# Performance work log

Measured on AMD Instinct MI355X. Metric: run time of the kernel, lower is better.

Reference implementation:

```python
import jax, jax.numpy as jnp
import numpy as np

B = 128          # batch of IQ signals
L = 128          # signal length
PL = 16          # patch length
ST = 4           # patch stride
WIN = 4          # local window
NPATCH = (L - PL) // ST + 1   # 29
HID = 256
NCLS = 8
NG = B * NPATCH               # number of patch graphs
N = NG * PL                   # total nodes


def _build_edges():
    src, dst = [], []
    for i in range(PL):
        for j in range(PL):
            if 0 < abs(i - j) <= WIN:
                src.append(i); dst.append(j)
    bs = np.array(src, np.int32)          # [108]
    bd = np.array(dst, np.int32)
    off = (np.arange(NG, dtype=np.int32) * PL)[:, None]
    isrc = (off + bs[None, :]).reshape(-1)
    idst = (off + bd[None, :]).reshape(-1)
    # cross-patch edges: last node of patch p -> first node of patch p+1
    b = np.arange(B, dtype=np.int32)[:, None]
    p = np.arange(NPATCH - 1, dtype=np.int32)[None, :]
    csrc = (b * NPATCH * PL + p * PL + (PL - 1)).reshape(-1)
    cdst = (b * NPATCH * PL + (p + 1) * PL).reshape(-1)
    return np.concatenate([isrc, csrc]), np.concatenate([idst, cdst])


def setup_inputs() -> dict:
    key = jax.random.key(0)
    ks = jax.random.split(key, 10)
    s = 0.05
    esrc, edst = _build_edges()
    return {
        "iq_signal": jax.random.normal(ks[0], (B, 2, L), jnp.float32),
        "edge_src": jnp.asarray(esrc),
        "edge_dst": jnp.asarray(edst),
        # SAGEConv layer 0 (in=2): lin_l (agg, with bias), lin_r (root, no bias)
        "W0_agg": jax.random.normal(ks[1], (HID, 2), jnp.float32) * s,
        "W0_root": jax.random.normal(ks[2], (HID, 2), jnp.float32) * s,
        "b0": jnp.zeros((HID,), jnp.float32),
        # SAGEConv layers 1..3 (256 -> 256), stacked
        "W_agg": jax.random.normal(ks[3], (3, HID, HID), jnp.float32) * s,
        "W_root": jax.random.normal(ks[4], (3, HID, HID), jnp.float32) * s,
        "b_lin": jnp.zeros((3, HID), jnp.float32),
        # per-layer LayerNorms
        "ln_scale": jnp.ones((4, HID), jnp.float32),
        "ln_bias": jnp.zeros((4, HID), jnp.float32),
        # classifier head
        "cls_W1": jax.random.normal(ks[5], (HID, HID), jnp.float32) * s,
        "cls_b1": jnp.zeros((HID,), jnp.float32),
        "cls_ln_scale": jnp.ones((HID,), jnp.float32),
        "cls_ln_bias": jnp.zeros((HID,), jnp.float32),
        "cls_W2": jax.random.normal(ks[6], (NCLS, HID), jnp.float32) * s,
        "cls_b2": jnp.zeros((NCLS,), jnp.float32),
    }


def _ln(x, g, b):
    m = x.mean(-1, keepdims=True)
    v = ((x - m) ** 2).mean(-1, keepdims=True)
    return (x - m) * jax.lax.rsqrt(v + 1e-5) * g + b


def reference(iq_signal, edge_src, edge_dst, W0_agg, W0_root, b0,
              W_agg, W_root, b_lin, ln_scale, ln_bias,
              cls_W1, cls_b1, cls_ln_scale, cls_ln_bias, cls_W2, cls_b2):
    # patch extraction: [B,2,L] -> [B,NPATCH,PL,2] -> node features [N,2]
    idx = jnp.arange(NPATCH)[:, None] * ST + jnp.arange(PL)[None, :]   # [29,16]
    x = jnp.transpose(iq_signal[:, :, idx], (0, 2, 3, 1)).reshape(-1, 2)

    # in-degree for mean aggregation (0 -> safe divide by 1)
    ones = jnp.ones((edge_dst.shape[0],), x.dtype)
    deg = jax.ops.segment_sum(ones, edge_dst, num_segments=N)
    inv_deg = 1.0 / jnp.maximum(deg, 1.0)

    def sage(h, Wa, Wr, b):
        # mean-aggregate neighbor messages, then lin_l(agg) + lin_r(h) + bias
        agg = jax.ops.segment_sum(h[edge_src], edge_dst, num_segments=N)
        agg = agg * inv_deg[:, None]
        return agg @ Wa.T + h @ Wr.T + b

    # layer 0 (2 -> 256): no residual (shape change)
    h = jax.nn.relu(_ln(sage(x, W0_agg, W0_root, b0), ln_scale[0], ln_bias[0]))
    # layers 1..3 with residual
    for l in range(3):
        hn = jax.nn.relu(_ln(sage(h, W_agg[l], W_root[l], b_lin[l]),
                             ln_scale[l + 1], ln_bias[l + 1]))
        h = h + hn

    node_emb = h                                  # [N, 256]
    # global_mean_pool per patch graph (16 consecutive nodes each)
    gf = node_emb.reshape(NG, PL, HID).mean(axis=1)   # [NG, 256]
    z = jax.nn.relu(_ln(gf @ cls_W1.T + cls_b1, cls_ln_scale, cls_ln_bias))
    logits = z @ cls_W2.T + cls_b2                # [NG, 8]
    return logits, gf, node_emb
```

## Files before the change

### kernel.cpp

```cpp
#include <hip/hip_runtime.h>
#include <hip/hip_bf16.h>

typedef __hip_bfloat16 bf16;
typedef unsigned short u16;
typedef unsigned int uint32;
typedef __attribute__((ext_vector_type(8))) short bf16x8;
typedef __attribute__((ext_vector_type(4))) float f32x4;

#define BATCH   128
#define LSIG    128
#define PL      16
#define ST      4
#define WIN     4
#define NPATCH  29
#define NG      (BATCH * NPATCH)
#define NNODE   (NG * PL)
#define HID     256
#define NCLS    8

#define IQ_OFF    0
#define W0A_OFF   32768
#define W0R_OFF   33280
#define B0_OFF    33792
#define BLIN_OFF  34048
#define LNS_OFF   34816
#define LNB_OFF   35840
#define W1T_OFF   36864
#define CB1_OFF   102400
#define CLNS_OFF  102656
#define CLNB_OFF  102912
#define CW2_OFF   103168
#define CB2_OFF   105216
#define CVT_TOTAL 105224

#define P_BYTE_OFF   4096
#define WB_BYTE_OFF  425984
#define A_BYTE_OFF   1216512
#define B_BYTE_OFF   1959936
#define GF_EOFF      (NG * NCLS)
#define EMB_EOFF     (NG * NCLS + NG * HID)

__device__ __forceinline__ float b2f(bf16 x) { return __bfloat162float(x); }
__device__ __forceinline__ float lof(uint32 u) { return __uint_as_float(u << 16); }
__device__ __forceinline__ float hif(uint32 u) { return __uint_as_float(u & 0xFFFF0000u); }
__device__ __forceinline__ float ldmix(const void* p, int i, int fl) {
  return fl ? ((const float*)p)[i] : __bfloat162float(((const bf16*)p)[i]);
}

__global__ __launch_bounds__(256) void detect_kernel(const u16* __restrict__ iq, int* flag) {
  __shared__ int sbig, snz;
  int t = threadIdx.x;
  if (t == 0) { sbig = 0; snz = 0; }
  __syncthreads();
  int big = 0, nz = 0;
  for (int e = t; e < 16384; e += 256) {
    u16 u = iq[2 * e];
    int ex = (u >> 7) & 0xFF;
    if (ex >= 0xC0) big++;
    if (u != 0) nz++;
  }
  atomicAdd(&sbig, big); atomicAdd(&snz, nz);
  __syncthreads();
  if (t == 0) *flag = (sbig > 4 || snz < 100) ? 1 : 0;
}

__global__ __launch_bounds__(256) void convert_params(
    const int* __restrict__ flag,
    const void* iq, const void* w0a, const void* w0r, const void* b0,
    const void* blin, const void* lns, const void* lnb,
    const void* cw1, const void* cb1, const void* clns, const void* clnb,
    const void* cw2, const void* cb2,
    float* __restrict__ P) {
  int idx = blockIdx.x * 256 + threadIdx.x;
  if (idx >= CVT_TOTAL) return;
  int fl = *flag;
  float v;
  if (idx < W0A_OFF)        v = ldmix(iq,  idx, fl);
  else if (idx < W0R_OFF)   v = ldmix(w0a, idx - W0A_OFF, fl);
  else if (idx < B0_OFF)    v = ldmix(w0r, idx - W0R_OFF, fl);
  else if (idx < BLIN_OFF)  v = ldmix(b0,  idx - B0_OFF, fl);
  else if (idx < LNS_OFF)   v = ldmix(blin, idx - BLIN_OFF, fl);
  else if (idx < LNB_OFF)   v = ldmix(lns, idx - LNS_OFF, fl);
  else if (idx < W1T_OFF)   v = ldmix(lnb, idx - LNB_OFF, fl);
  else if (idx < CB1_OFF) { int t2 = idx - W1T_OFF;
    v = ldmix(cw1, (t2 & 255) * 256 + (t2 >> 8), fl); }
  else if (idx < CLNS_OFF)  v = ldmix(cb1, idx - CB1_OFF, fl);
  else if (idx < CLNB_OFF)  v = ldmix(clns, idx - CLNS_OFF, fl);
  else if (idx < CW2_OFF)   v = ldmix(clnb, idx - CLNB_OFF, fl);
  else if (idx < CB2_OFF)   v = ldmix(cw2, idx - CW2_OFF, fl);
  else                      v = ldmix(cb2, idx - CB2_OFF, fl);
  P[idx] = v;
}

__global__ __launch_bounds__(256) void convert_wb(
    const int* __restrict__ flag, const void* wag, const void* wro, bf16* __restrict__ WB) {
  int idx = blockIdx.x * 256 + threadIdx.x;
  int fl = *flag;
  int l = idx >> 17, m = (idx >> 16) & 1, r = idx & 65535;
  const void* src = m ? wro : wag;
  WB[idx] = __float2bfloat16(ldmix(src, l * 65536 + r, fl));
}

__global__ __launch_bounds__(256) void layer0_kernel(
    const float* __restrict__ P, bf16* __restrict__ hout) {
  int g = blockIdx.x, f = threadIdx.x;
  int b = g / NPATCH, p = g % NPATCH;
  __shared__ float x_s[PL][2];
  __shared__ float xp_s[2];
  __shared__ float agg_s[PL][2];
  __shared__ float o_s[PL][HID];
  __shared__ float mv_s[PL][2];
  if (f < 32) { int j = f & 15, c = f >> 4;
    x_s[j][c] = P[IQ_OFF + (b * 2 + c) * LSIG + p * ST + j]; }
  if (f < 2) xp_s[f] = (p > 0) ? P[IQ_OFF + (b * 2 + f) * LSIG + (p - 1) * ST + PL - 1] : 0.f;
  __syncthreads();
  if (f < 32) { int j = f & 15, c = f >> 4;
    float s = 0.f;
    int lo = j - WIN < 0 ? 0 : j - WIN, hi = j + WIN > 15 ? 15 : j + WIN;
    for (int i = lo; i <= hi; ++i) if (i != j) s += x_s[i][c];
    int deg = (j < WIN ? j : WIN) + ((15 - j) < WIN ? (15 - j) : WIN);
    if (j == 0 && p > 0) { s += xp_s[c]; deg += 1; }
    agg_s[j][c] = s / (float)deg;
  }
  __syncthreads();
  float wa0 = P[W0A_OFF + f * 2], wa1 = P[W0A_OFF + f * 2 + 1];
  float wr0 = P[W0R_OFF + f * 2], wr1 = P[W0R_OFF + f * 2 + 1];
  float bb = P[B0_OFF + f];
#pragma unroll
  for (int j = 0; j < PL; ++j)
    o_s[j][f] = agg_s[j][0] * wa0 + agg_s[j][1] * wa1 + x_s[j][0] * wr0 + x_s[j][1] * wr1 + bb;
  __syncthreads();
  { int j = f >> 4, q = f & 15;
    float s = 0.f, s2 = 0.f;
#pragma unroll
    for (int i = 0; i < 16; ++i) { float v = o_s[j][q + 16 * i]; s += v; s2 += v * v; }
#pragma unroll
    for (int m = 8; m >= 1; m >>= 1) { s += __shfl_xor(s, m); s2 += __shfl_xor(s2, m); }
    if (q == 0) { float mean = s * (1.f / HID);
      float var = s2 * (1.f / HID) - mean * mean;
      mv_s[j][0] = mean; mv_s[j][1] = rsqrtf(var + 1e-5f); }
  }
  __syncthreads();
  float gl = P[LNS_OFF + f], bl = P[LNB_OFF + f];
#pragma unroll
  for (int j = 0; j < PL; ++j) {
    float v = (o_s[j][f] - mv_s[j][0]) * mv_s[j][1] * gl + bl;
    v = v > 0.f ? v : 0.f;
    hout[(size_t)(g * PL + j) * HID + f] = __float2bfloat16(v);
  }
}

#define MFMA_BF16 __builtin_amdgcn_mfma_f32_16x16x32_bf16
__global__ __launch_bounds__(256, 2) void sage_mfma(
    const bf16* __restrict__ hin,
    const bf16* __restrict__ Wa, const bf16* __restrict__ Wr,
    const float* __restrict__ bias,
    const float* __restrict__ lng, const float* __restrict__ lnb,
    bf16* __restrict__ hout) {
  int t = threadIdx.x;
  int w = t >> 6, l = t & 63, lr = l & 15, lg = l >> 4;
  int g0 = blockIdx.x * 4;
  size_t nbase = (size_t)g0 * PL;
  __shared__ uint32 h32[64 * 128];
  __shared__ uint32 a32[64 * 128];
  float* mvp = (float*)h32;
  const uint32* hinw = (const uint32*)hin;

  int colbase = w * 64;
  const bf16* waB = Wa + (colbase + lr) * HID + lg * 8;
  const bf16* wrB = Wr + (colbase + lr) * HID + lg * 8;
  bf16x8 wa0[2][8], wr0[2][8];
#pragma unroll
  for (int nt = 0; nt < 2; ++nt)
#pragma unroll
    for (int ks = 0; ks < 8; ++ks) {
      wa0[nt][ks] = *(const bf16x8*)(waB + nt * 16 * HID + ks * 32);
      wr0[nt][ks] = *(const bf16x8*)(wrB + nt * 16 * HID + ks * 32);
    }

  const uint32* hg = hinw + nbase * 128;
#pragma unroll
  for (int it = 0; it < 8; ++it) {
    int u = it * 256 + t;
    int row = u >> 5, sl = u & 31;
    int sw = sl ^ (row & 7);
    *(uint4*)&h32[row * 128 + sw * 4] = *(const uint4*)(hg + u * 4);
  }
  __syncthreads();

  {
    int c2 = t & 127, Ph = t >> 7;
#pragma unroll
    for (int pi = 0; pi < 2; ++pi) {
      int pp = Ph + pi * 2;
      int pr = pp * 16;
      int hp = ((g0 + pp) % NPATCH) != 0;
      float vlo[16], vhi[16];
#pragma unroll
      for (int j = 0; j < 16; ++j) {
        uint32 u = h32[(pr + j) * 128 + (((c2 >> 2) ^ (j & 7)) << 2) + (c2 & 3)];
        vlo[j] = lof(u); vhi[j] = hif(u);
      }
      float blo = 0.f, bhi = 0.f;
      if (hp) {
        uint32 u;
        if (pp == 0) u = hinw[(nbase - 1) * 128 + c2];
        else { int br = pr - 1;
          u = a32[0];
          u = h32[br * 128 + (((c2 >> 2) ^ (br & 7)) << 2) + (c2 & 3)]; }
        blo = lof(u); bhi = hif(u);
      }
#pragma unroll
      for (int j = 0; j < 16; ++j) {
        const int a = (j - WIN < 0) ? 0 : j - WIN;
        const int b = (j + WIN > 15) ? 15 : j + WIN;
        float slo = 0.f, shi = 0.f;
#pragma unroll
        for (int i = 0; i < 16; ++i)
          if (i >= a && i <= b && i != j) { slo += vlo[i]; shi += vhi[i]; }
        float deg = (float)((j < WIN ? j : WIN) + (15 - j < WIN ? 15 - j : WIN));
        if (j == 0 && hp) { slo += blo; shi += bhi; deg += 1.f; }
        float inv = 1.f / deg;
        bf16 r0 = __float2bfloat16(slo * inv), r1 = __float2bfloat16(shi * inv);
        uint32 wv = ((uint32)(*(const u16*)&r1) << 16) | (uint32)(*(const u16*)&r0);
        a32[(pr + j) * 128 + (((c2 >> 2) ^ (j & 7)) << 2) + (c2 & 3)] = wv;
      }
    }
  }
  __syncthreads();

  f32x4 acc[4][4];
#pragma unroll
  for (int m = 0; m < 4; ++m)
#pragma unroll
    for (int n = 0; n < 4; ++n) acc[m][n] = (f32x4){0.f, 0.f, 0.f, 0.f};
#pragma unroll
  for (int ks = 0; ks < 8; ++ks) {
    bf16x8 wa1[2], wr1[2];
#pragma unroll
    for (int nt = 0; nt < 2; ++nt) {
      wa1[nt] = *(const bf16x8*)(waB + (nt + 2) * 16 * HID + ks * 32);
      wr1[nt] = *(const bf16x8*)(wrB + (nt + 2) * 16 * HID + ks * 32);
    }
#pragma unroll
    for (int m = 0; m < 4; ++m) {
      int row = m * 16 + lr;
      int idx = row * 128 + ((((ks * 4 + lg) ^ (lr & 7))) << 2);
      bf16x8 af = *(const bf16x8*)&a32[idx];
      bf16x8 hf = *(const bf16x8*)&h32[idx];
      acc[m][0] = MFMA_BF16(af, wa0[0][ks], acc[m][0], 0, 0, 0);
      acc[m][0] = MFMA_BF16(hf, wr0[0][ks], acc[m][0], 0, 0, 0);
      acc[m][1] = MFMA_BF16(af, wa0[1][ks], acc[m][1], 0, 0, 0);
      acc[m][1] = MFMA_BF16(hf, wr0[1][ks], acc[m][1], 0, 0, 0);
      acc[m][2] = MFMA_BF16(af, wa1[0],     acc[m][2], 0, 0, 0);
      acc[m][2] = MFMA_BF16(hf, wr1[0],     acc[m][2], 0, 0, 0);
      acc[m][3] = MFMA_BF16(af, wa1[1],     acc[m][3], 0, 0, 0);
      acc[m][3] = MFMA_BF16(hf, wr1[1],     acc[m][3], 0, 0, 0);
    }
  }
#pragma unroll
  for (int nt = 0; nt < 4; ++nt) {
    float bv = bias[colbase + nt * 16 + lr];
#pragma unroll
    for (int m = 0; m < 4; ++m) {
      acc[m][nt][0] += bv; acc[m][nt][1] += bv;
      acc[m][nt][2] += bv; acc[m][nt][3] += bv;
    }
  }
  __syncthreads();

#pragma unroll
  for (int m = 0; m < 4; ++m)
#pragma unroll
    for (int nt = 0; nt < 4; ++nt) {
      int col = colbase + nt * 16 + lr;
#pragma unroll
      for (int r = 0; r < 4; ++r) {
        int row = m * 16 + lg * 4 + r;
        int i16 = row * 256 + (((col >> 3) ^ (row & 7)) << 3) + (col & 7);
        bf16 x = __float2bfloat16(acc[m][nt][r]);
        ((u16*)a32)[i16] = *(const u16*)&x;
      }
    }
  __syncthreads();

  {
    int row = t >> 2, q = t & 3;
    float s = 0.f, s2 = 0.f;
#pragma unroll
    for (int i = 0; i < 32; ++i) {
      int d = q * 32 + i;
      uint32 u = a32[row * 128 + (((d >> 2) ^ (row & 7)) << 2) + (d & 3)];
      float a = lof(u), b = hif(u);
      s += a + b; s2 += a * a + b * b;
    }
    s += __shfl_xor(s, 1); s2 += __shfl_xor(s2, 1);
    s += __shfl_xor(s, 2); s2 += __shfl_xor(s2, 2);
    if (q == 0) { float mean = s * (1.f / HID);
      mvp[row * 2] = mean;
      mvp[row * 2 + 1] = rsqrtf(s2 * (1.f / HID) - mean * mean + 1e-5f); }
  }
  __syncthreads();

  {
    int c2 = t & 127, part = t >> 7;
    float gl0 = lng[c2 * 2], gl1 = lng[c2 * 2 + 1];
    float bl0 = lnb[c2 * 2], bl1 = lnb[c2 * 2 + 1];
    uint32* outw = (uint32*)hout + nbase * 128;
    const uint32* inw = hinw + nbase * 128;
#pragma unroll
    for (int i = 0; i < 32; ++i) {
      int row = part * 32 + i;
      uint32 u = a32[row * 128 + (((c2 >> 2) ^ (row & 7)) << 2) + (c2 & 3)];
      float mean = mvp[row * 2], rstd = mvp[row * 2 + 1];
      float a = (lof(u) - mean) * rstd * gl0 + bl0; a = a > 0.f ? a : 0.f;
      float b = (hif(u) - mean) * rstd * gl1 + bl1; b = b > 0.f ? b : 0.f;
      uint32 hu = inw[row * 128 + c2];
      a += lof(hu); b += hif(hu);
      bf16 r0 = __float2bfloat16(a), r1 = __float2bfloat16(b);
      uint32 wv = ((uint32)(*(const u16*)&r1) << 16) | (uint32)(*(const u16*)&r0);
      outw[row * 128 + c2] = wv;
    }
  }
}

__global__ __launch_bounds__(256) void head_kernel(
    const bf16* __restrict__ emb, const float* __restrict__ P,
    void* __restrict__ dout, const int* __restrict__ flag) {
  int g = blockIdx.x, f = threadIdx.x;
  int fl = *flag;
  __shared__ float gf_s[HID];
  __shared__ float z_s[HID];
  __shared__ float ps[4], ps2[4];
  __shared__ float mr[2];
  const bf16* eb = emb + (size_t)g * PL * HID;
  float s = 0.f;
#pragma unroll
  for (int r = 0; r < PL; ++r) s += b2f(eb[r * HID + f]);
  s *= (1.f / PL);
  gf_s[f] = s;
  { size_t ei = (size_t)GF_EOFF + (size_t)g * HID + f;
    if (fl) ((float*)dout)[ei] = s; else ((bf16*)dout)[ei] = __float2bfloat16(s); }
  __syncthreads();
  float acc = P[CB1_OFF + f];
  for (int k = 0; k < HID; k += 4) {
    const float4 gv = *(const float4*)(&gf_s[k]);
    acc = fmaf(gv.x, P[W1T_OFF + (k + 0) * HID + f], acc);
    acc = fmaf(gv.y, P[W1T_OFF + (k + 1) * HID + f], acc);
    acc = fmaf(gv.z, P[W1T_OFF + (k + 2) * HID + f], acc);
    acc = fmaf(gv.w, P[W1T_OFF + (k + 3) * HID + f], acc);
  }
  float s1 = acc, s2 = acc * acc;
#pragma unroll
  for (int m = 32; m >= 1; m >>= 1) { s1 += __shfl_xor(s1, m); s2 += __shfl_xor(s2, m); }
  int wid = f >> 6, lane = f & 63;
  if (lane == 0) { ps[wid] = s1; ps2[wid] = s2; }
  __syncthreads();
  if (f == 0) {
    float S = ps[0] + ps[1] + ps[2] + ps[3];
    float S2 = ps2[0] + ps2[1] + ps2[2] + ps2[3];
    float mean = S * (1.f / HID);
    mr[0] = mean; mr[1] = rsqrtf(S2 * (1.f / HID) - mean * mean + 1e-5f);
  }
  __syncthreads();
  float z = (acc - mr[0]) * mr[1] * P[CLNS_OFF + f] + P[CLNB_OFF + f];
  z = z > 0.f ? z : 0.f;
  z_s[f] = z;
  __syncthreads();
  if (f < NCLS) {
    float a = P[CB2_OFF + f];
    for (int k = 0; k < HID; ++k) a = fmaf(z_s[k], P[CW2_OFF + f * HID + k], a);
    size_t ei = (size_t)g * NCLS + f;
    if (fl) ((float*)dout)[ei] = a; else ((bf16*)dout)[ei] = __float2bfloat16(a);
  }
}

__global__ __launch_bounds__(256) void emit_emb(
    const bf16* __restrict__ A, void* __restrict__ dout, const int* __restrict__ flag) {
  int fl = *flag;
  size_t n = (size_t)NNODE * HID;
  for (size_t i = blockIdx.x * 256ull + threadIdx.x; i < n; i += 2048ull * 256ull) {
    bf16 v = A[i];
    size_t ei = (size_t)EMB_EOFF + i;
    if (fl) ((float*)dout)[ei] = b2f(v); else ((bf16*)dout)[ei] = v;
  }
}

extern "C" void kernel_launch(void* const* d_in, const int* in_sizes, int n_in,
                              void* d_out, int out_size, void* d_ws, size_t ws_size,
                              hipStream_t stream) {
  char* ws = (char*)d_ws;
  int*   flag = (int*)ws;
  float* P    = (float*)(ws + P_BYTE_OFF);
  bf16*  WB   = (bf16*)(ws + WB_BYTE_OFF);
  bf16*  A    = (bf16*)(ws + A_BYTE_OFF);
  bf16*  B    = (bf16*)((char*)d_out + B_BYTE_OFF);

  detect_kernel<<<1, 256, 0, stream>>>((const u16*)d_in[0], flag);
  convert_params<<<(CVT_TOTAL + 255) / 256, 256, 0, stream>>>(
      flag, d_in[0], d_in[3], d_in[4], d_in[5], d_in[8],
      d_in[9], d_in[10], d_in[11], d_in[12], d_in[13], d_in[14], d_in[15], d_in[16], P);
  convert_wb<<<1536, 256, 0, stream>>>(flag, d_in[6], d_in[7], WB);

  layer0_kernel<<<NG, 256, 0, stream>>>(P, B);
  sage_mfma<<<NG / 4, 256, 0, stream>>>(B, WB, WB + 65536,
      P + BLIN_OFF, P + LNS_OFF + HID, P + LNB_OFF + HID, A);
  sage_mfma<<<NG / 4, 256, 0, stream>>>(A, WB + 131072, WB + 131072 + 65536,
      P + BLIN_OFF + HID, P + LNS_OFF + 2 * HID, P + LNB_OFF + 2 * HID, B);
  sage_mfma<<<NG / 4, 256, 0, stream>>>(B, WB + 262144, WB + 262144 + 65536,
      P + BLIN_OFF + 2 * HID, P + LNS_OFF + 3 * HID, P + LNB_OFF + 3 * HID, A);
  head_kernel<<<NG, 256, 0, stream>>>(A, P, d_out, flag);
  emit_emb<<<2048, 256, 0, stream>>>(A, d_out, flag);
}
```

Measured before the change: 238.0 us.

## Fuse layer0 into first SAGE kernel and fold pooling/emb output into last layer

Layer 0 is recomputed inside the first SAGE block, so its 256-wide activations never round-trip through global memory. The last SAGE layer writes node embeddings and per-patch mean pooling straight to the output, which removes the emit_emb pass and the pooling step in the head kernel. The SAGE kernel now uses one shared buffer: it runs the root GEMM first, overwrites the buffer in place with the sliding-window aggregation, then runs the aggregate GEMM. LayerNorm statistics come from accumulator registers via shuffles, and occupancy is raised to 4 blocks per CU. The trade-off is weight fragments reloaded per k-step instead of held in registers, plus extra layer-0 recompute in the epilogue.

```diff
diff --git a/kernel.cpp b/kernel.cpp
--- a/kernel.cpp
+++ b/kernel.cpp
@@ -40,10 +40,16 @@
 #define GF_EOFF      (NG * NCLS)
 #define EMB_EOFF     (NG * NCLS + NG * HID)
 
+#define MFMA_BF16 __builtin_amdgcn_mfma_f32_16x16x32_bf16
+
 __device__ __forceinline__ float b2f(bf16 x) { return __bfloat162float(x); }
 __device__ __forceinline__ float lof(uint32 u) { return __uint_as_float(u << 16); }
 __device__ __forceinline__ float hif(uint32 u) { return __uint_as_float(u & 0xFFFF0000u); }
-__device__ __forceinline__ float ldmix(const void* p, int i, int fl) {
+__device__ __forceinline__ uint32 packbf(float a, float b) {
+  bf16 r0 = __float2bfloat16(a), r1 = __float2bfloat16(b);
+  return ((uint32)(*(const u16*)&r1) << 16) | (uint32)(*(const u16*)&r0);
+}
+__device__ __forceinline__ float ldmix(const void* p, size_t i, int fl) {
   return fl ? ((const float*)p)[i] : __bfloat162float(((const bf16*)p)[i]);
 }
 
@@ -101,174 +107,249 @@
   WB[idx] = __float2bfloat16(ldmix(src, l * 65536 + r, fl));
 }
 
-__global__ __launch_bounds__(256) void layer0_kernel(
-    const float* __restrict__ P, bf16* __restrict__ hout) {
-  int g = blockIdx.x, f = threadIdx.x;
-  int b = g / NPATCH, p = g % NPATCH;
-  __shared__ float x_s[PL][2];
-  __shared__ float xp_s[2];
-  __shared__ float agg_s[PL][2];
-  __shared__ float o_s[PL][HID];
-  __shared__ float mv_s[PL][2];
-  if (f < 32) { int j = f & 15, c = f >> 4;
-    x_s[j][c] = P[IQ_OFF + (b * 2 + c) * LSIG + p * ST + j]; }
-  if (f < 2) xp_s[f] = (p > 0) ? P[IQ_OFF + (b * 2 + f) * LSIG + (p - 1) * ST + PL - 1] : 0.f;
-  __syncthreads();
-  if (f < 32) { int j = f & 15, c = f >> 4;
-    float s = 0.f;
-    int lo = j - WIN < 0 ? 0 : j - WIN, hi = j + WIN > 15 ? 15 : j + WIN;
-    for (int i = lo; i <= hi; ++i) if (i != j) s += x_s[i][c];
-    int deg = (j < WIN ? j : WIN) + ((15 - j) < WIN ? (15 - j) : WIN);
-    if (j == 0 && p > 0) { s += xp_s[c]; deg += 1; }
-    agg_s[j][c] = s / (float)deg;
-  }
-  __syncthreads();
-  float wa0 = P[W0A_OFF + f * 2], wa1 = P[W0A_OFF + f * 2 + 1];
-  float wr0 = P[W0R_OFF + f * 2], wr1 = P[W0R_OFF + f * 2 + 1];
-  float bb = P[B0_OFF + f];
-#pragma unroll
-  for (int j = 0; j < PL; ++j)
-    o_s[j][f] = agg_s[j][0] * wa0 + agg_s[j][1] * wa1 + x_s[j][0] * wr0 + x_s[j][1] * wr1 + bb;
-  __syncthreads();
-  { int j = f >> 4, q = f & 15;
-    float s = 0.f, s2 = 0.f;
-#pragma unroll
-    for (int i = 0; i < 16; ++i) { float v = o_s[j][q + 16 * i]; s += v; s2 += v * v; }
-#pragma unroll
-    for (int m = 8; m >= 1; m >>= 1) { s += __shfl_xor(s, m); s2 += __shfl_xor(s2, m); }
-    if (q == 0) { float mean = s * (1.f / HID);
-      float var = s2 * (1.f / HID) - mean * mean;
-      mv_s[j][0] = mean; mv_s[j][1] = rsqrtf(var + 1e-5f); }
-  }
-  __syncthreads();
-  float gl = P[LNS_OFF + f], bl = P[LNB_OFF + f];
-#pragma unroll
-  for (int j = 0; j < PL; ++j) {
-    float v = (o_s[j][f] - mv_s[j][0]) * mv_s[j][1] * gl + bl;
-    v = v > 0.f ? v : 0.f;
-    hout[(size_t)(g * PL + j) * HID + f] = __float2bfloat16(v);
-  }
-}
-
-#define MFMA_BF16 __builtin_amdgcn_mfma_f32_16x16x32_bf16
-__global__ __launch_bounds__(256, 2) void sage_mfma(
+template<int FUSED, int LAST>
+__global__ __launch_bounds__(256, 4) void sage_k(
     const bf16* __restrict__ hin,
+    const float* __restrict__ P,
     const bf16* __restrict__ Wa, const bf16* __restrict__ Wr,
     const float* __restrict__ bias,
     const float* __restrict__ lng, const float* __restrict__ lnb,
-    bf16* __restrict__ hout) {
+    bf16* __restrict__ hout,
+    void* __restrict__ dout,
+    const int* __restrict__ flag) {
   int t = threadIdx.x;
-  int w = t >> 6, l = t & 63, lr = l & 15, lg = l >> 4;
   int g0 = blockIdx.x * 4;
   size_t nbase = (size_t)g0 * PL;
-  __shared__ uint32 h32[64 * 128];
-  __shared__ uint32 a32[64 * 128];
-  float* mvp = (float*)h32;
+  __shared__ uint32 hb[65 * 128];
+  __shared__ float part_s[64][4][2];
+  __shared__ float mv_s[64][2];
+  __shared__ float x_s[65][2];
+  __shared__ float ag_s[65][2];
+  __shared__ float mv0[65][2];
+  __shared__ float xb_s[5][2];
+  int hp0 = (g0 % NPATCH) != 0;
   const uint32* hinw = (const uint32*)hin;
 
+  if constexpr (FUSED) {
+    if (t < 128) {
+      int pp = t >> 5, j = (t >> 1) & 15, c = t & 1;
+      int gid = g0 + pp, b = gid / NPATCH, p = gid % NPATCH;
+      x_s[pp * 16 + j][c] = P[IQ_OFF + (b * 2 + c) * LSIG + p * ST + j];
+    } else if (t < 138) {
+      if (hp0) {
+        int q = t - 128, j = 11 + (q >> 1), c = q & 1;
+        int gid = g0 - 1, b = gid / NPATCH, p = gid % NPATCH;
+        xb_s[j - 11][c] = P[IQ_OFF + (b * 2 + c) * LSIG + p * ST + j];
+      }
+    }
+    __syncthreads();
+    if (t < 2) {
+      if (hp0) {
+        x_s[64][t] = xb_s[4][t];
+        ag_s[64][t] = (xb_s[0][t] + xb_s[1][t] + xb_s[2][t] + xb_s[3][t]) * 0.25f;
+      } else { x_s[64][t] = 0.f; ag_s[64][t] = 0.f; }
+    }
+    if (t < 128) {
+      int pp = t >> 5, j = (t >> 1) & 15, c = t & 1;
+      int gid = g0 + pp; int hp = (gid % NPATCH) != 0;
+      int lo = j - 4 < 0 ? 0 : j - 4, hi = j + 4 > 15 ? 15 : j + 4;
+      float s = 0.f;
+      for (int i = lo; i <= hi; ++i) if (i != j) s += x_s[pp * 16 + i][c];
+      float deg = (float)((j < 4 ? j : 4) + (15 - j < 4 ? 15 - j : 4));
+      if (j == 0 && hp) { s += (pp == 0) ? xb_s[4][c] : x_s[pp * 16 - 1][c]; deg += 1.f; }
+      ag_s[pp * 16 + j][c] = s / deg;
+    }
+    __syncthreads();
+    {
+      int r = t >> 2, fc = (t & 3) * 64;
+      float xs0 = x_s[r][0], xs1 = x_s[r][1], as0 = ag_s[r][0], as1 = ag_s[r][1];
+      float s = 0.f, s2 = 0.f;
+#pragma unroll
+      for (int i = 0; i < 64; i += 2) {
+        int f = fc + i;
+        float2 wa = *(const float2*)&P[W0A_OFF + f * 2];
+        float2 wr = *(const float2*)&P[W0R_OFF + f * 2];
+        float2 wa2 = *(const float2*)&P[W0A_OFF + f * 2 + 2];
+        float2 wr2 = *(const float2*)&P[W0R_OFF + f * 2 + 2];
+        float2 bb = *(const float2*)&P[B0_OFF + f];
+        float o0 = as0 * wa.x + as1 * wa.y + xs0 * wr.x + xs1 * wr.y + bb.x;
+        float o1 = as0 * wa2.x + as1 * wa2.y + xs0 * wr2.x + xs1 * wr2.y + bb.y;
+        s += o0 + o1; s2 += o0 * o0 + o1 * o1;
+        int d = f >> 1;
+        hb[r * 128 + (((d >> 2) ^ (r & 7)) << 2) + (d & 3)] = packbf(o0, o1);
+      }
+      s += __shfl_xor(s, 1); s2 += __shfl_xor(s2, 1);
+      s += __shfl_xor(s, 2); s2 += __shfl_xor(s2, 2);
+      float mean = s * (1.f / HID);
+      float rstd = rsqrtf(s2 * (1.f / HID) - mean * mean + 1e-5f);
+      if ((t & 3) == 0) { mv0[r][0] = mean; mv0[r][1] = rstd; }
+#pragma unroll
+      for (int i = 0; i < 32; ++i) {
+        int d = (fc >> 1) + i;
+        int idx = r * 128 + (((d >> 2) ^ (r & 7)) << 2) + (d & 3);
+        uint32 u = hb[idx];
+        int f = d * 2;
+        float a = (lof(u) - mean) * rstd * P[LNS_OFF + f] + P[LNB_OFF + f];
+        float b_ = (hif(u) - mean) * rstd * P[LNS_OFF + f + 1] + P[LNB_OFF + f + 1];
+        a = a > 0.f ? a : 0.f; b_ = b_ > 0.f ? b_ : 0.f;
+        hb[idx] = packbf(a, b_);
+      }
+      if (t < 4 && hp0) {
+        int fc4 = t * 64;
+        float bx0 = x_s[64][0], bx1 = x_s[64][1], ba0 = ag_s[64][0], ba1 = ag_s[64][1];
+        float bs = 0.f, bs2 = 0.f;
+#pragma unroll
+        for (int i = 0; i < 64; i += 2) {
+          int f = fc4 + i;
+          float2 wa = *(const float2*)&P[W0A_OFF + f * 2];
+          float2 wr = *(const float2*)&P[W0R_OFF + f * 2];
+          float2 wa2 = *(const float2*)&P[W0A_OFF + f * 2 + 2];
+          float2 wr2 = *(const float2*)&P[W0R_OFF + f * 2 + 2];
+          float2 bb = *(const float2*)&P[B0_OFF + f];
+          float o0 = ba0 * wa.x + ba1 * wa.y + bx0 * wr.x + bx1 * wr.y + bb.x;
+          float o1 = ba0 * wa2.x + ba1 * wa2.y + bx0 * wr2.x + bx1 * wr2.y + bb.y;
+          bs += o0 + o1; bs2 += o0 * o0 + o1 * o1;
+          int d = f >> 1;
+          hb[64 * 128 + d] = packbf(o0, o1);
+        }
+        bs += __shfl_xor(bs, 1); bs2 += __shfl_xor(bs2, 1);
+        bs += __shfl_xor(bs, 2); bs2 += __shfl_xor(bs2, 2);
+        float mean = bs * (1.f / HID);
+        float rstd = rsqrtf(bs2 * (1.f / HID) - mean * mean + 1e-5f);
+        if (t == 0) { mv0[64][0] = mean; mv0[64][1] = rstd; }
+#pragma unroll
+        for (int i = 0; i < 32; ++i) {
+          int d = (fc4 >> 1) + i;
+          uint32 u = hb[64 * 128 + d];
+          int f = d * 2;
+          float a = (lof(u) - mean) * rstd * P[LNS_OFF + f] + P[LNB_OFF + f];
+          float b_ = (hif(u) - mean) * rstd * P[LNS_OFF + f + 1] + P[LNB_OFF + f + 1];
+          a = a > 0.f ? a : 0.f; b_ = b_ > 0.f ? b_ : 0.f;
+          hb[64 * 128 + d] = packbf(a, b_);
+        }
+      }
+    }
+    __syncthreads();
+  } else {
+    const uint32* hg = hinw + nbase * 128;
+#pragma unroll
+    for (int it = 0; it < 8; ++it) {
+      int u = it * 256 + t;
+      int row = u >> 5, sl = u & 31;
+      *(uint4*)&hb[row * 128 + ((sl ^ (row & 7)) << 2)] = *(const uint4*)(hg + u * 4);
+    }
+    if (t < 32) {
+      uint4 v = make_uint4(0u, 0u, 0u, 0u);
+      if (hp0) v = *(const uint4*)(hg - 128 + t * 4);
+      *(uint4*)&hb[64 * 128 + (t << 2)] = v;
+    }
+    __syncthreads();
+  }
+
+  int w = t >> 6, l = t & 63, lr = l & 15, lg = l >> 4;
   int colbase = w * 64;
+  f32x4 acc[4][4];
+#pragma unroll
+  for (int m = 0; m < 4; ++m)
+#pragma unroll
+    for (int n = 0; n < 4; ++n) acc[m][n] = (f32x4){0.f, 0.f, 0.f, 0.f};
+  const bf16* wrB = Wr + (colbase + lr) * HID + lg * 8;
+#pragma unroll
+  for (int ks = 0; ks < 8; ++ks) {
+    bf16x8 bfr[4];
+#pragma unroll
+    for (int nt = 0; nt < 4; ++nt) bfr[nt] = *(const bf16x8*)(wrB + nt * 16 * HID + ks * 32);
+#pragma unroll
+    for (int m = 0; m < 4; ++m) {
+      bf16x8 af = *(const bf16x8*)&hb[(m * 16 + lr) * 128 + (((ks * 4 + lg) ^ (lr & 7)) << 2)];
+#pragma unroll
+      for (int nt = 0; nt < 4; ++nt) acc[m][nt] = MFMA_BF16(af, bfr[nt], acc[m][nt], 0, 0, 0);
+    }
+  }
+
+  int pp = t >> 6, cc = t & 63;
+  int hpp = ((g0 + pp) % NPATCH) != 0;
+  int brow = (pp == 0) ? 64 : (pp * 16 - 1);
+  uint32 bndA = 0, bndB = 0;
+  if (hpp) {
+    bndA = hb[brow * 128 + (((cc >> 2) ^ (brow & 7)) << 2) + (cc & 3)];
+    int cb = cc + 64;
+    bndB = hb[brow * 128 + (((cb >> 2) ^ (brow & 7)) << 2) + (cb & 3)];
+  }
+  __syncthreads();
+  {
+    const float INV1[16] = {0.25f, 0.2f, 1.f/6.f, 1.f/7.f,
+                            0.125f, 0.125f, 0.125f, 0.125f, 0.125f, 0.125f, 0.125f, 0.125f,
+                            1.f/7.f, 1.f/6.f, 0.2f, 0.25f};
+    int pr = pp * 16;
+#pragma unroll
+    for (int half = 0; half < 2; ++half) {
+      int c2 = cc + half * 64;
+      uint32 bnd = half ? bndB : bndA;
+      uint32 v[16];
+#pragma unroll
+      for (int j = 0; j < 16; ++j)
+        v[j] = hb[(pr + j) * 128 + (((c2 >> 2) ^ (j & 7)) << 2) + (c2 & 3)];
+      float wlo = 0.f, whi = 0.f;
+#pragma unroll
+      for (int j = 0; j < 5; ++j) { wlo += lof(v[j]); whi += hif(v[j]); }
+#pragma unroll
+      for (int j = 0; j < 16; ++j) {
+        float slo = wlo - lof(v[j]);
+        float shi = whi - hif(v[j]);
+        float inv = INV1[j];
+        if (j == 0 && hpp) { slo += lof(bnd); shi += hif(bnd); inv = 0.2f; }
+        hb[(pr + j) * 128 + (((c2 >> 2) ^ (j & 7)) << 2) + (c2 & 3)] = packbf(slo * inv, shi * inv);
+        if (j < 11) { wlo += lof(v[j + 5]); whi += hif(v[j + 5]); }
+        if (j >= 4) { wlo -= lof(v[j - 4]); whi -= hif(v[j - 4]); }
+      }
+    }
+  }
+  __syncthreads();
+
   const bf16* waB = Wa + (colbase + lr) * HID + lg * 8;
-  const bf16* wrB = Wr + (colbase + lr) * HID + lg * 8;
-  bf16x8 wa0[2][8], wr0[2][8];
-#pragma unroll
-  for (int nt = 0; nt < 2; ++nt)
-#pragma unroll
-    for (int ks = 0; ks < 8; ++ks) {
-      wa0[nt][ks] = *(const bf16x8*)(waB + nt * 16 * HID + ks * 32);
-      wr0[nt][ks] = *(const bf16x8*)(wrB + nt * 16 * HID + ks * 32);
-    }
-
-  const uint32* hg = hinw + nbase * 128;
-#pragma unroll
-  for (int it = 0; it < 8; ++it) {
-    int u = it * 256 + t;
-    int row = u >> 5, sl = u & 31;
-    int sw = sl ^ (row & 7);
-    *(uint4*)&h32[row * 128 + sw * 4] = *(const uint4*)(hg + u * 4);
-  }
-  __syncthreads();
-
-  {
-    int c2 = t & 127, Ph = t >> 7;
-#pragma unroll
-    for (int pi = 0; pi < 2; ++pi) {
-      int pp = Ph + pi * 2;
-      int pr = pp * 16;
-      int hp = ((g0 + pp) % NPATCH) != 0;
-      float vlo[16], vhi[16];
-#pragma unroll
-      for (int j = 0; j < 16; ++j) {
-        uint32 u = h32[(pr + j) * 128 + (((c2 >> 2) ^ (j & 7)) << 2) + (c2 & 3)];
-        vlo[j] = lof(u); vhi[j] = hif(u);
-      }
-      float blo = 0.f, bhi = 0.f;
-      if (hp) {
-        uint32 u;
-        if (pp == 0) u = hinw[(nbase - 1) * 128 + c2];
-        else { int br = pr - 1;
-          u = a32[0];
-          u = h32[br * 128 + (((c2 >> 2) ^ (br & 7)) << 2) + (c2 & 3)]; }
-        blo = lof(u); bhi = hif(u);
-      }
-#pragma unroll
-      for (int j = 0; j < 16; ++j) {
-        const int a = (j - WIN < 0) ? 0 : j - WIN;
-        const int b = (j + WIN > 15) ? 15 : j + WIN;
-        float slo = 0.f, shi = 0.f;
-#pragma unroll
-        for (int i = 0; i < 16; ++i)
-          if (i >= a && i <= b && i != j) { slo += vlo[i]; shi += vhi[i]; }
-        float deg = (float)((j < WIN ? j : WIN) + (15 - j < WIN ? 15 - j : WIN));
-        if (j == 0 && hp) { slo += blo; shi += bhi; deg += 1.f; }
-        float inv = 1.f / deg;
-        bf16 r0 = __float2bfloat16(slo * inv), r1 = __float2bfloat16(shi * inv);
-        uint32 wv = ((uint32)(*(const u16*)&r1) << 16) | (uint32)(*(const u16*)&r0);
-        a32[(pr + j) * 128 + (((c2 >> 2) ^ (j & 7)) << 2) + (c2 & 3)] = wv;
-      }
-    }
-  }
-  __syncthreads();
-
-  f32x4 acc[4][4];
-#pragma unroll
-  for (int m = 0; m < 4; ++m)
-#pragma unroll
-    for (int n = 0; n < 4; ++n) acc[m][n] = (f32x4){0.f, 0.f, 0.f, 0.f};
 #pragma unroll
   for (int ks = 0; ks < 8; ++ks) {
-    bf16x8 wa1[2], wr1[2];
-#pragma unroll
-    for (int nt = 0; nt < 2; ++nt) {
-      wa1[nt] = *(const bf16x8*)(waB + (nt + 2) * 16 * HID + ks * 32);
-      wr1[nt] = *(const bf16x8*)(wrB + (nt + 2) * 16 * HID + ks * 32);
-    }
+    bf16x8 bfa[4];
+#pragma unroll
+    for (int nt = 0; nt < 4; ++nt) bfa[nt] = *(const bf16x8*)(waB + nt * 16 * HID + ks * 32);
 #pragma unroll
     for (int m = 0; m < 4; ++m) {
-      int row = m * 16 + lr;
-      int idx = row * 128 + ((((ks * 4 + lg) ^ (lr & 7))) << 2);
-      bf16x8 af = *(const bf16x8*)&a32[idx];
-      bf16x8 hf = *(const bf16x8*)&h32[idx];
-      acc[m][0] = MFMA_BF16(af, wa0[0][ks], acc[m][0], 0, 0, 0);
-      acc[m][0] = MFMA_BF16(hf, wr0[0][ks], acc[m][0], 0, 0, 0);
-      acc[m][1] = MFMA_BF16(af, wa0[1][ks], acc[m][1], 0, 0, 0);
-      acc[m][1] = MFMA_BF16(hf, wr0[1][ks], acc[m][1], 0, 0, 0);
-      acc[m][2] = MFMA_BF16(af, wa1[0],     acc[m][2], 0, 0, 0);
-      acc[m][2] = MFMA_BF16(hf, wr1[0],     acc[m][2], 0, 0, 0);
-      acc[m][3] = MFMA_BF16(af, wa1[1],     acc[m][3], 0, 0, 0);
-      acc[m][3] = MFMA_BF16(hf, wr1[1],     acc[m][3], 0, 0, 0);
-    }
-  }
+      bf16x8 af = *(const bf16x8*)&hb[(m * 16 + lr) * 128 + (((ks * 4 + lg) ^ (lr & 7)) << 2)];
+#pragma unroll
+      for (int nt = 0; nt < 4; ++nt) acc[m][nt] = MFMA_BF16(af, bfa[nt], acc[m][nt], 0, 0, 0);
+    }
+  }
+
 #pragma unroll
   for (int nt = 0; nt < 4; ++nt) {
     float bv = bias[colbase + nt * 16 + lr];
 #pragma unroll
     for (int m = 0; m < 4; ++m) {
-      acc[m][nt][0] += bv; acc[m][nt][1] += bv;
-      acc[m][nt][2] += bv; acc[m][nt][3] += bv;
-    }
-  }
-  __syncthreads();
-
+      acc[m][nt][0] += bv; acc[m][nt][1] += bv; acc[m][nt][2] += bv; acc[m][nt][3] += bv;
+    }
+  }
+#pragma unroll
+  for (int m = 0; m < 4; ++m)
+#pragma unroll
+    for (int r = 0; r < 4; ++r) {
+      float s = acc[m][0][r] + acc[m][1][r] + acc[m][2][r] + acc[m][3][r];
+      float s2 = acc[m][0][r] * acc[m][0][r] + acc[m][1][r] * acc[m][1][r]
+               + acc[m][2][r] * acc[m][2][r] + acc[m][3][r] * acc[m][3][r];
+      s += __shfl_xor(s, 1); s2 += __shfl_xor(s2, 1);
+      s += __shfl_xor(s, 2); s2 += __shfl_xor(s2, 2);
+      s += __shfl_xor(s, 4); s2 += __shfl_xor(s2, 4);
+      s += __shfl_xor(s, 8); s2 += __shfl_xor(s2, 8);
+      if (lr == 0) { int row = m * 16 + lg * 4 + r; part_s[row][w][0] = s; part_s[row][w][1] = s2; }
+    }
+  __syncthreads();
+  if (t < 64) {
+    float S = part_s[t][0][0] + part_s[t][1][0] + part_s[t][2][0] + part_s[t][3][0];
+    float S2 = part_s[t][0][1] + part_s[t][1][1] + part_s[t][2][1] + part_s[t][3][1];
+    float mean = S * (1.f / HID);
+    mv_s[t][0] = mean;
+    mv_s[t][1] = rsqrtf(S2 * (1.f / HID) - mean * mean + 1e-5f);
+  }
 #pragma unroll
   for (int m = 0; m < 4; ++m)
 #pragma unroll
@@ -277,55 +358,84 @@
 #pragma unroll
       for (int r = 0; r < 4; ++r) {
         int row = m * 16 + lg * 4 + r;
-        int i16 = row * 256 + (((col >> 3) ^ (row & 7)) << 3) + (col & 7);
         bf16 x = __float2bfloat16(acc[m][nt][r]);
-        ((u16*)a32)[i16] = *(const u16*)&x;
+        ((u16*)hb)[row * 256 + (((col >> 3) ^ (row & 7)) << 3) + (col & 7)] = *(const u16*)&x;
       }
     }
   __syncthreads();
 
   {
-    int row = t >> 2, q = t & 3;
-    float s = 0.f, s2 = 0.f;
-#pragma unroll
-    for (int i = 0; i < 32; ++i) {
-      int d = q * 32 + i;
-      uint32 u = a32[row * 128 + (((d >> 2) ^ (row & 7)) << 2) + (d & 3)];
-      float a = lof(u), b = hif(u);
-      s += a + b; s2 += a * a + b * b;
-    }
-    s += __shfl_xor(s, 1); s2 += __shfl_xor(s2, 1);
-    s += __shfl_xor(s, 2); s2 += __shfl_xor(s2, 2);
-    if (q == 0) { float mean = s * (1.f / HID);
-      mvp[row * 2] = mean;
-      mvp[row * 2 + 1] = rsqrtf(s2 * (1.f / HID) - mean * mean + 1e-5f); }
-  }
-  __syncthreads();
-
-  {
-    int c2 = t & 127, part = t >> 7;
+    int c2 = t & 127, prt = t >> 7;
     float gl0 = lng[c2 * 2], gl1 = lng[c2 * 2 + 1];
     float bl0 = lnb[c2 * 2], bl1 = lnb[c2 * 2 + 1];
-    uint32* outw = (uint32*)hout + nbase * 128;
+    float2 fwa0, fwa1, fwr0, fwr1;
+    float fb0 = 0, fb1 = 0, fg0 = 0, fg1 = 0, fbb0 = 0, fbb1 = 0;
+    if constexpr (FUSED) {
+      fwa0 = *(const float2*)&P[W0A_OFF + c2 * 4];
+      fwa1 = *(const float2*)&P[W0A_OFF + c2 * 4 + 2];
+      fwr0 = *(const float2*)&P[W0R_OFF + c2 * 4];
+      fwr1 = *(const float2*)&P[W0R_OFF + c2 * 4 + 2];
+      fb0 = P[B0_OFF + c2 * 2]; fb1 = P[B0_OFF + c2 * 2 + 1];
+      fg0 = P[LNS_OFF + c2 * 2]; fg1 = P[LNS_OFF + c2 * 2 + 1];
+      fbb0 = P[LNB_OFF + c2 * 2]; fbb1 = P[LNB_OFF + c2 * 2 + 1];
+    }
+    int fl = 0;
+    if constexpr (LAST) fl = *flag;
+    uint32* outw = nullptr;
     const uint32* inw = hinw + nbase * 128;
-#pragma unroll
-    for (int i = 0; i < 32; ++i) {
-      int row = part * 32 + i;
-      uint32 u = a32[row * 128 + (((c2 >> 2) ^ (row & 7)) << 2) + (c2 & 3)];
-      float mean = mvp[row * 2], rstd = mvp[row * 2 + 1];
-      float a = (lof(u) - mean) * rstd * gl0 + bl0; a = a > 0.f ? a : 0.f;
-      float b = (hif(u) - mean) * rstd * gl1 + bl1; b = b > 0.f ? b : 0.f;
-      uint32 hu = inw[row * 128 + c2];
-      a += lof(hu); b += hif(hu);
-      bf16 r0 = __float2bfloat16(a), r1 = __float2bfloat16(b);
-      uint32 wv = ((uint32)(*(const u16*)&r1) << 16) | (uint32)(*(const u16*)&r0);
-      outw[row * 128 + c2] = wv;
+    if constexpr (!LAST) outw = (uint32*)hout + nbase * 128;
+#pragma unroll
+    for (int pi = 0; pi < 2; ++pi) {
+      float sga = 0.f, sgb = 0.f;
+#pragma unroll
+      for (int i = 0; i < 16; ++i) {
+        int row = prt * 32 + pi * 16 + i;
+        uint32 u = hb[row * 128 + (((c2 >> 2) ^ (row & 7)) << 2) + (c2 & 3)];
+        float mean = mv_s[row][0], rstd = mv_s[row][1];
+        float a = (lof(u) - mean) * rstd * gl0 + bl0; a = a > 0.f ? a : 0.f;
+        float b_ = (hif(u) - mean) * rstd * gl1 + bl1; b_ = b_ > 0.f ? b_ : 0.f;
+        float h0a, h0b;
+        if constexpr (FUSED) {
+          float o0 = ag_s[row][0] * fwa0.x + ag_s[row][1] * fwa0.y
+                   + x_s[row][0] * fwr0.x + x_s[row][1] * fwr0.y + fb0;
+          float o1 = ag_s[row][0] * fwa1.x + ag_s[row][1] * fwa1.y
+                   + x_s[row][0] * fwr1.x + x_s[row][1] * fwr1.y + fb1;
+          float m0 = mv0[row][0], r0 = mv0[row][1];
+          h0a = (o0 - m0) * r0 * fg0 + fbb0; h0a = h0a > 0.f ? h0a : 0.f;
+          h0b = (o1 - m0) * r0 * fg1 + fbb1; h0b = h0b > 0.f ? h0b : 0.f;
+        } else {
+          uint32 hu = inw[row * 128 + c2];
+          h0a = lof(hu); h0b = hif(hu);
+        }
+        a += h0a; b_ += h0b;
+        if constexpr (!LAST) {
+          outw[row * 128 + c2] = packbf(a, b_);
+        } else {
+          sga += a; sgb += b_;
+          if (fl) {
+            size_t ei = (size_t)EMB_EOFF + (nbase + row) * 256 + c2 * 2;
+            ((float*)dout)[ei] = a; ((float*)dout)[ei + 1] = b_;
+          } else {
+            ((uint32*)dout)[(EMB_EOFF >> 1) + (nbase + row) * 128 + c2] = packbf(a, b_);
+          }
+        }
+      }
+      if constexpr (LAST) {
+        float ga = sga * (1.f / PL), gb = sgb * (1.f / PL);
+        int gidx = g0 + prt * 2 + pi;
+        if (fl) {
+          size_t gi = (size_t)GF_EOFF + (size_t)gidx * 256 + c2 * 2;
+          ((float*)dout)[gi] = ga; ((float*)dout)[gi + 1] = gb;
+        } else {
+          ((uint32*)dout)[(GF_EOFF >> 1) + gidx * 128 + c2] = packbf(ga, gb);
+        }
+      }
     }
   }
 }
 
 __global__ __launch_bounds__(256) void head_kernel(
-    const bf16* __restrict__ emb, const float* __restrict__ P,
+    const void* __restrict__ gin, const float* __restrict__ P,
     void* __restrict__ dout, const int* __restrict__ flag) {
   int g = blockIdx.x, f = threadIdx.x;
   int fl = *flag;
@@ -333,14 +443,8 @@
   __shared__ float z_s[HID];
   __shared__ float ps[4], ps2[4];
   __shared__ float mr[2];
-  const bf16* eb = emb + (size_t)g * PL * HID;
-  float s = 0.f;
-#pragma unroll
-  for (int r = 0; r < PL; ++r) s += b2f(eb[r * HID + f]);
-  s *= (1.f / PL);
-  gf_s[f] = s;
-  { size_t ei = (size_t)GF_EOFF + (size_t)g * HID + f;
-    if (fl) ((float*)dout)[ei] = s; else ((bf16*)dout)[ei] = __float2bfloat16(s); }
+  gf_s[f] = fl ? ((const float*)gin)[(size_t)GF_EOFF + (size_t)g * HID + f]
+               : b2f(((const bf16*)gin)[(size_t)GF_EOFF + (size_t)g * HID + f]);
   __syncthreads();
   float acc = P[CB1_OFF + f];
   for (int k = 0; k < HID; k += 4) {
@@ -372,17 +476,6 @@
     for (int k = 0; k < HID; ++k) a = fmaf(z_s[k], P[CW2_OFF + f * HID + k], a);
     size_t ei = (size_t)g * NCLS + f;
     if (fl) ((float*)dout)[ei] = a; else ((bf16*)dout)[ei] = __float2bfloat16(a);
-  }
-}
-
-__global__ __launch_bounds__(256) void emit_emb(
-    const bf16* __restrict__ A, void* __restrict__ dout, const int* __restrict__ flag) {
-  int fl = *flag;
-  size_t n = (size_t)NNODE * HID;
-  for (size_t i = blockIdx.x * 256ull + threadIdx.x; i < n; i += 2048ull * 256ull) {
-    bf16 v = A[i];
-    size_t ei = (size_t)EMB_EOFF + i;
-    if (fl) ((float*)dout)[ei] = b2f(v); else ((bf16*)dout)[ei] = v;
   }
 }
 
@@ -402,13 +495,11 @@
       d_in[9], d_in[10], d_in[11], d_in[12], d_in[13], d_in[14], d_in[15], d_in[16], P);
   convert_wb<<<1536, 256, 0, stream>>>(flag, d_in[6], d_in[7], WB);
 
-  layer0_kernel<<<NG, 256, 0, stream>>>(P, B);
-  sage_mfma<<<NG / 4, 256, 0, stream>>>(B, WB, WB + 65536,
-      P + BLIN_OFF, P + LNS_OFF + HID, P + LNB_OFF + HID, A);
-  sage_mfma<<<NG / 4, 256, 0, stream>>>(A, WB + 131072, WB + 131072 + 65536,
-      P + BLIN_OFF + HID, P + LNS_OFF + 2 * HID, P + LNB_OFF + 2 * HID, B);
-  sage_mfma<<<NG / 4, 256, 0, stream>>>(B, WB + 262144, WB + 262144 + 65536,
-      P + BLIN_OFF + 2 * HID, P + LNS_OFF + 3 * HID, P + LNB_OFF + 3 * HID, A);
-  head_kernel<<<NG, 256, 0, stream>>>(A, P, d_out, flag);
-  emit_emb<<<2048, 256, 0, stream>>>(A, d_out, flag);
-}
+  sage_k<1, 0><<<NG / 4, 256, 0, stream>>>(nullptr, P, WB, WB + 65536,
+      P + BLIN_OFF, P + LNS_OFF + HID, P + LNB_OFF + HID, B, nullptr, flag);
+  sage_k<0, 0><<<NG / 4, 256, 0, stream>>>(B, P, WB + 131072, WB + 131072 + 65536,
+      P + BLIN_OFF + HID, P + LNS_OFF + 2 * HID, P + LNB_OFF + 2 * HID, A, nullptr, flag);
+  sage_k<0, 1><<<NG / 4, 256, 0, stream>>>(A, P, WB + 262144, WB + 262144 + 65536,
+      P + BLIN_OFF + 2 * HID, P + LNS_OFF + 3 * HID, P + LNB_OFF + 3 * HID, nullptr, d_out, flag);
+  head_kernel<<<NG, 256, 0, stream>>>(d_out, P, d_out, flag);
+}
```

Result: slower. 290.8 us (+22.2%).
